# Optimization experiments

Hardware: AMD Instinct MI355X
Metric: run time of the kernel (lower is better)

## Reference

```python
import jax, jax.numpy as jnp
import numpy as np

N_HEADS = 16


def setup_inputs() -> dict:
    key = jax.random.key(0)
    ks = jax.random.split(key, 8)
    B, S, E = 4, 2048, 1024
    s = 0.02
    return {
        "input_tensor": jax.random.normal(ks[0], (B, S, E), jnp.float32),
        "mask": jnp.zeros((B, 1, 1, S), jnp.float32),  # additive mask (0 = keep)
        "WQ_w": jax.random.normal(ks[1], (E, E), jnp.float32) * s,
        "WQ_b": jnp.zeros((E,), jnp.float32),
        "WK_w": jax.random.normal(ks[2], (E, E), jnp.float32) * s,
        "WK_b": jnp.zeros((E,), jnp.float32),
        "WV_w": jax.random.normal(ks[3], (E, E), jnp.float32) * s,
        "WV_b": jnp.zeros((E,), jnp.float32),
        "WO_w": jax.random.normal(ks[4], (E, E), jnp.float32) * s,
        "WO_b": jnp.zeros((E,), jnp.float32),
        "ln_w": jnp.ones((E,), jnp.float32),
        "ln_b": jnpp if False else jnp.zeros((E,), jnp.float32),
    }


def reference(input_tensor, mask, WQ_w, WQ_b, WK_w, WK_b, WV_w, WV_b,
              WO_w, WO_b, ln_w, ln_b):
    B, S, E = input_tensor.shape
    H = N_HEADS
    D = E // H
    scale = jnp.sqrt(jnp.asarray(D, input_tensor.dtype))

    def split_heads(x):  # [B,S,E] -> [B,H,S,D]
        return x.reshape(B, S, H, D).transpose(0, 2, 1, 3)

    q = split_heads(input_tensor @ WQ_w.T + WQ_b)
    k = split_heads(input_tensor @ WK_w.T + WK_b)
    v = split_heads(input_tensor @ WV_w.T + WV_b)

    scores = jnp.einsum("bhqd,bhkd->bhqk", q, k) / scale + mask
    probs = jax.nn.softmax(scores, axis=-1)  # attn dropout is identity in eval
    ctx = jnp.einsum("bhqk,bhkd->bhqd", probs, v)
    ctx = ctx.transpose(0, 2, 1, 3).reshape(B, S, E)

    out = ctx @ WO_w.T + WO_b  # out dropout is identity in eval
    x = input_tensor + out
    mu = jnp.mean(x, axis=-1, keepdims=True)
    var = jnp.var(x, axis=-1, keepdims=True)
    eps = 1e-12
    return (x - mu) * jax.lax.rsqrt(var + eps) * ln_w + ln_b
```

## Files before the change

### kernel.cpp

```cpp
#include <hip/hip_runtime.h>
#include <hip/hip_bf16.h>
#include <stdint.h>


typedef short bf16x8_t __attribute__((ext_vector_type(8)));
typedef float f32x4_t __attribute__((ext_vector_type(4)));
typedef float f32x16_t __attribute__((ext_vector_type(16)));
typedef unsigned short u16x8_t __attribute__((ext_vector_type(8)));
typedef uint32_t u32x4_t __attribute__((ext_vector_type(4)));

#define DEV static __device__ __forceinline__

DEV unsigned short f2bf(float f) {
  union { float f; uint32_t u; } v; v.f = f;
  uint32_t u = v.u;
  return (unsigned short)((u + 0x7fffu + ((u >> 16) & 1u)) >> 16);
}

DEV uint32_t cvtpk(float a, float b) {
  uint32_t d;
  asm("v_cvt_pk_bf16_f32 %0, %1, %2" : "=v"(d) : "v"(a), "v"(b));
  return d;
}

DEV void plswap(uint32_t& a, uint32_t& b) {
  asm("v_permlane32_swap_b32 %0, %1" : "+v"(a), "+v"(b));
}

DEV float ex2(float x) { return __builtin_amdgcn_exp2f(x); }

template<int N> DEV void wait_vm() {
  asm volatile("s_waitcnt vmcnt(%0)" :: "n"(N) : "memory");
}
DEV void bar() { __builtin_amdgcn_s_barrier(); }
DEV void sbar0() { __builtin_amdgcn_sched_barrier(0); }

typedef const __attribute__((address_space(1))) void* gp_t;
typedef __attribute__((address_space(3))) void* lp_t;

DEV void gld16(const void* g, void* l) {
  __builtin_amdgcn_global_load_lds((gp_t)g, (lp_t)l, 16, 0, 0);
}

__global__ __launch_bounds__(256) void cast_all(
    const float* __restrict__ x,
    const float* __restrict__ wq, const float* __restrict__ wk,
    const float* __restrict__ wv, const float* __restrict__ wo,
    const float* __restrict__ mask,
    unsigned short* __restrict__ xb,
    unsigned short* __restrict__ wqb, unsigned short* __restrict__ wkb,
    unsigned short* __restrict__ wvb, unsigned short* __restrict__ wob,
    float* __restrict__ emf, unsigned short* __restrict__ emb)
{
  const int cid = blockIdx.x;
  if (cid >= 6144) {
    int i = ((cid - 6144) * 256 + (int)threadIdx.x) * 8;
    float4 a = *(const float4*)(mask + i);
    float4 b = *(const float4*)(mask + i + 4);
    const float C = 1.44269504f;
    float4 ea, eb;
    ea.x = ex2(a.x * C); ea.y = ex2(a.y * C); ea.z = ex2(a.z * C); ea.w = ex2(a.w * C);
    eb.x = ex2(b.x * C); eb.y = ex2(b.y * C); eb.z = ex2(b.z * C); eb.w = ex2(b.w * C);
    *(float4*)(emf + i) = ea;
    *(float4*)(emf + i + 4) = eb;
    u16x8_t o;
    o[0] = f2bf(ea.x); o[1] = f2bf(ea.y); o[2] = f2bf(ea.z); o[3] = f2bf(ea.w);
    o[4] = f2bf(eb.x); o[5] = f2bf(eb.y); o[6] = f2bf(eb.z); o[7] = f2bf(eb.w);
    *(u16x8_t*)(emb + i) = o;
    return;
  }
  const float* src; unsigned short* dst; int base;
  if (cid < 4096)      { src = x;  dst = xb;  base = cid; }
  else if (cid < 4608) { src = wq; dst = wqb; base = cid - 4096; }
  else if (cid < 5120) { src = wk; dst = wkb; base = cid - 4608; }
  else if (cid < 5632) { src = wv; dst = wvb; base = cid - 5120; }
  else                 { src = wo; dst = wob; base = cid - 5632; }
  int i = (base * 256 + (int)threadIdx.x) * 8;
  float4 a = *(const float4*)(src + i);
  float4 b = *(const float4*)(src + i + 4);
  u16x8_t o;
  o[0] = f2bf(a.x); o[1] = f2bf(a.y); o[2] = f2bf(a.z); o[3] = f2bf(a.w);
  o[4] = f2bf(b.x); o[5] = f2bf(b.y); o[6] = f2bf(b.z); o[7] = f2bf(b.w);
  *(u16x8_t*)(dst + i) = o;
}

template<int MODE>
__global__ __launch_bounds__(256) void gemm_bt(
    const unsigned short* __restrict__ A,
    const unsigned short* __restrict__ B0, const unsigned short* __restrict__ B1,
    const float* __restrict__ bias0, const float* __restrict__ bias1,
    const float* __restrict__ resid,
    unsigned short* __restrict__ o0, unsigned short* __restrict__ o1,
    float* __restrict__ of,
    int M, int N, int K)
{
  __shared__ unsigned short As[2][128 * 32];
  __shared__ unsigned short Bs[2][128 * 32];

  const int z = blockIdx.z;
  const unsigned short* Bw = (MODE == 0 && z == 1) ? B1 : B0;
  const float* bias = (MODE == 0 && z == 1) ? bias1 : bias0;
  unsigned short* obf = (MODE == 0 && z == 1) ? o1 : o0;

  const int tid = threadIdx.x;
  const int lane = tid & 63;
  const int lr = lane & 15, lq = lane >> 4;
  const int wid = tid >> 6;
  const int m0 = blockIdx.x * 128;
  const int n0 = blockIdx.y * 128;
  const int wr = (wid >> 1) * 64, wc = (wid & 1) * 64;

  f32x4_t acc[4][4] = {};

  const int o = tid * 16;
  const int srow = o >> 6, scb = o & 63;

  auto STAGE = [&](int kt, int p) {
#pragma unroll
    for (int r = 0; r < 2; ++r) {
      int row = srow + r * 64;
      int oo = o + r * 4096;
      gld16((const char*)(A  + (size_t)(m0 + row) * K + kt) + scb, (char*)As[p] + oo);
      gld16((const char*)(Bw + (size_t)(n0 + row) * K + kt) + scb, (char*)Bs[p] + oo);
    }
  };

  STAGE(0, 0);
  wait_vm<0>();
  bar(); sbar0();

  int cur = 0;
  for (int kt = 32; kt <= K; kt += 32) {
    if (kt < K) {
      STAGE(kt, cur ^ 1);
      wait_vm<4>();
    } else {
      wait_vm<0>();
    }
    bar(); sbar0();

    bf16x8_t aF[4], bF[4];
    const int koff = lq * 16;
#pragma unroll
    for (int i = 0; i < 4; ++i) {
      aF[i] = *(const bf16x8_t*)((const char*)As[cur] + (wr + i * 16 + lr) * 64 + koff);
      bF[i] = *(const bf16x8_t*)((const char*)Bs[cur] + (wc + i * 16 + lr) * 64 + koff);
    }
#pragma unroll
    for (int i = 0; i < 4; ++i)
#pragma unroll
      for (int j = 0; j < 4; ++j)
        acc[i][j] = __builtin_amdgcn_mfma_f32_16x16x32_bf16(aF[i], bF[j], acc[i][j], 0, 0, 0);

    bar();
    cur ^= 1;
  }

#pragma unroll
  for (int i = 0; i < 4; ++i) {
#pragma unroll
    for (int j = 0; j < 4; ++j) {
      int n = n0 + wc + j * 16 + lr;
#pragma unroll
      for (int r = 0; r < 4; ++r) {
        int m = m0 + wr + i * 16 + lq * 4 + r;
        float v = acc[i][j][r];
        if (MODE == 0) {
          v = (v + bias[n]) * (z == 0 ? 0.18033688f : 1.0f);
          int b = m >> 11, s = m & 2047, h = n >> 6, d = n & 63;
          obf[(size_t)((b * 16 + h) * 2048 + s) * 64 + d] = f2bf(v);
        } else if (MODE == 2) {
          v = (v + bias[m]) * resid[n];
          int b = n >> 11, s = n & 2047;
          obf[(size_t)(b * 1024 + m) * 2048 + s] = f2bf(v);
        } else {
          v = v + bias[n] + resid[(size_t)m * 1024 + n];
          of[(size_t)m * 1024 + n] = v;
        }
      }
    }
  }
}

__global__ __launch_bounds__(256, 2) void attn_kernel(
    const unsigned short* __restrict__ Qg, const unsigned short* __restrict__ Kg,
    const unsigned short* __restrict__ Vtg, const unsigned short* __restrict__ EMb,
    unsigned short* __restrict__ ctx)
{
  __shared__ __align__(16) char smem[69632];

  const int id = blockIdx.x;
  const int swz = (id & 7) * 64 + (id >> 3);
  const int bh = swz >> 3, qt = swz & 7;
  const int b = bh >> 4, h = bh & 15;

  const int tid = threadIdx.x, lane = tid & 63, wid = tid >> 6;
  const int l31 = lane & 31, hi = lane >> 5;
  const int q0 = qt * 256 + wid * 64;
  const size_t head = (size_t)bh * (2048 * 64);
  const unsigned short* Kh = Kg + head;
  const unsigned short* Vh = Vtg + (size_t)bh * 64 * 2048;
  const unsigned short* emrow = EMb + (size_t)b * 2048;

  bf16x8_t qf[2][4];
#pragma unroll
  for (int qg = 0; qg < 2; ++qg) {
    const unsigned short* qp = Qg + head + (size_t)(q0 + qg * 32 + l31) * 64 + 8 * hi;
#pragma unroll
    for (int ds = 0; ds < 4; ++ds) qf[qg][ds] = *(const bf16x8_t*)(qp + ds * 16);
  }

  f32x16_t oaccA[2] = {}, oaccB[2] = {};
  f32x16_t lacc[2] = {};

  const int sw_row = (l31 & 7) << 4;

  auto STAGE = [&](int t, int p) {
    const int k0 = t * 128;
    char* kd = smem + p * 16384;
    char* vd = smem + 32768 + p * 16384;
#pragma unroll
    for (int r = 0; r < 4; ++r) {
      int oo = tid * 16 + r * 4096;
      {
        int row = oo >> 7, cb = oo & 127;
        int scb = cb ^ ((row & 7) << 4);
        gld16((const char*)(Kh + (size_t)(k0 + row) * 64) + scb, kd + oo);
      }
      {
        int row = oo >> 8, cb = oo & 255;
        int scb = cb ^ ((row & 7) << 4);
        gld16((const char*)(Vh + (size_t)row * 2048 + k0) + scb, vd + oo);
      }
    }
  };

  gld16((const char*)(emrow + tid * 8), smem + 65536 + tid * 16);
  STAGE(0, 0);
  wait_vm<0>();
  bar(); sbar0();

  for (int t = 0; t < 16; ++t) {
    const int p = t & 1;
    if (t < 15) {
      STAGE(t + 1, p ^ 1);
      wait_vm<8>();
    } else {
      wait_vm<0>();
    }
    bar(); sbar0();

    const char* kb = smem + p * 16384;
    const char* vb = smem + 32768 + p * 16384;
    const char* eb = smem + 65536 + t * 256;

#pragma unroll
    for (int s = 0; s < 2; ++s) {
      f32x16_t c0[2] = {}, c1[2] = {};
      {
        const char* kr0 = kb + s * 8192 + l31 * 128;
        const char* kr1 = kb + s * 8192 + (32 + l31) * 128;
        __builtin_amdgcn_s_setprio(1);
#pragma unroll
        for (int ds = 0; ds < 4; ++ds) {
          int cc = (ds * 32 + 16 * hi) ^ sw_row;
          bf16x8_t k0f = *(const bf16x8_t*)(kr0 + cc);
          bf16x8_t k1f = *(const bf16x8_t*)(kr1 + cc);
#pragma unroll
          for (int qg = 0; qg < 2; ++qg) {
            c0[qg] = __builtin_amdgcn_mfma_f32_32x32x16_bf16(k0f, qf[qg][ds], c0[qg], 0, 0, 0);
            c1[qg] = __builtin_amdgcn_mfma_f32_32x32x16_bf16(k1f, qf[qg][ds], c1[qg], 0, 0, 0);
          }
        }
        __builtin_amdgcn_s_setprio(0);
      }

      bf16x8_t pf[2][4];
#pragma unroll
      for (int qg = 0; qg < 2; ++qg) {
        uint32_t w0[8], w1[8];
#pragma unroll
        for (int g = 0; g < 8; ++g) {
          const int i4 = (g & 3) * 4;
          if (g < 4) {
            w0[g] = cvtpk(ex2(c0[qg][i4]), ex2(c0[qg][i4 + 1]));
            w1[g] = cvtpk(ex2(c0[qg][i4 + 2]), ex2(c0[qg][i4 + 3]));
          } else {
            w0[g] = cvtpk(ex2(c1[qg][i4]), ex2(c1[qg][i4 + 1]));
            w1[g] = cvtpk(ex2(c1[qg][i4 + 2]), ex2(c1[qg][i4 + 3]));
          }
        }
#pragma unroll
        for (int ks = 0; ks < 4; ++ks) {
          const int gg = ((ks >> 1) << 2) + ((ks & 1) << 1);
          uint32_t a0 = w0[gg], b0 = w0[gg + 1];
          uint32_t a1 = w1[gg], b1 = w1[gg + 1];
          plswap(a0, b0);
          plswap(a1, b1);
          union { uint32_t u[4]; bf16x8_t v; } cv;
          cv.u[0] = a0; cv.u[1] = a1; cv.u[2] = b0; cv.u[3] = b1;
          pf[qg][ks] = cv.v;
        }
      }

      {
        const char* vr0 = vb + l31 * 256 + s * 128;
        const char* vr1 = vb + (32 + l31) * 256 + s * 128;
        const char* ebs = eb + s * 128;
        __builtin_amdgcn_s_setprio(1);
#pragma unroll
        for (int ks = 0; ks < 4; ++ks) {
          bf16x8_t ef = *(const bf16x8_t*)(ebs + ks * 32 + 16 * hi);
          int cc = (ks * 32 + 16 * hi) ^ sw_row;
          bf16x8_t v0f = *(const bf16x8_t*)(vr0 + cc);
          bf16x8_t v1f = *(const bf16x8_t*)(vr1 + cc);
#pragma unroll
          for (int qg = 0; qg < 2; ++qg) {
            oaccA[qg] = __builtin_amdgcn_mfma_f32_32x32x16_bf16(v0f, pf[qg][ks], oaccA[qg], 0, 0, 0);
            oaccB[qg] = __builtin_amdgcn_mfma_f32_32x32x16_bf16(v1f, pf[qg][ks], oaccB[qg], 0, 0, 0);
            lacc[qg]  = __builtin_amdgcn_mfma_f32_32x32x16_bf16(ef,  pf[qg][ks], lacc[qg],  0, 0, 0);
          }
        }
        __builtin_amdgcn_s_setprio(0);
      }
    }
    bar();
  }

  char* tb = smem + wid * 8192;
#pragma unroll
  for (int qg = 0; qg < 2; ++qg) {
    const float inv = 1.0f / lacc[qg][0];
    char* trow = tb + qg * 4096 + l31 * 128;
    const int swq = (l31 & 7) << 4;
#pragma unroll
    for (int g2 = 0; g2 < 4; ++g2) {
      uint2 a0, a1;
      a0.x = cvtpk(oaccA[qg][4 * g2] * inv, oaccA[qg][4 * g2 + 1] * inv);
      a0.y = cvtpk(oaccA[qg][4 * g2 + 2] * inv, oaccA[qg][4 * g2 + 3] * inv);
      a1.x = cvtpk(oaccB[qg][4 * g2] * inv, oaccB[qg][4 * g2 + 1] * inv);
      a1.y = cvtpk(oaccB[qg][4 * g2 + 2] * inv, oaccB[qg][4 * g2 + 3] * inv);
      int d0 = 16 * g2 + 8 * hi;
      *(uint2*)(trow + ((d0) ^ swq)) = a0;
      *(uint2*)(trow + ((d0 + 64) ^ swq)) = a1;
    }
  }
#pragma unroll
  for (int half = 0; half < 2; ++half) {
    const int qq = half * 32 + (lane >> 1), cp = lane & 1;
    const char* trow = tb + qq * 128;
    const int swr = (qq & 7) << 4;
    unsigned short* op = ctx + ((size_t)(b * 2048 + q0 + qq)) * 1024 + h * 64 + cp * 32;
#pragma unroll
    for (int i = 0; i < 4; ++i) {
      int col = cp * 64 + i * 16;
      u32x4_t val = *(const u32x4_t*)(trow + (col ^ swr));
      *(u32x4_t*)(op + i * 8) = val;
    }
  }
}

__global__ __launch_bounds__(256) void ln_kernel(
    float* __restrict__ y, const float* __restrict__ g, const float* __restrict__ be)
{
  const int row = blockIdx.x, tid = threadIdx.x;
  float* rp = y + (size_t)row * 1024;
  float4 x = *(const float4*)(rp + tid * 4);
  float s = x.x + x.y + x.z + x.w;
  float sq = x.x * x.x + x.y * x.y + x.z * x.z + x.w * x.w;
#pragma unroll
  for (int msk = 1; msk < 64; msk <<= 1) {
    s  += __shfl_xor(s, msk);
    sq += __shfl_xor(sq, msk);
  }
  __shared__ float red[8];
  const int wid = tid >> 6, lane = tid & 63;
  if (lane == 0) { red[wid] = s; red[4 + wid] = sq; }
  __syncthreads();
  s  = red[0] + red[1] + red[2] + red[3];
  sq = red[4] + red[5] + red[6] + red[7];
  float mu = s * (1.f / 1024.f);
  float var = sq * (1.f / 1024.f) - mu * mu;
  float rs = rsqrtf(var + 1e-12f);
  float4 gw = *(const float4*)(g + tid * 4);
  float4 bw = *(const float4*)(be + tid * 4);
  float4 o2;
  o2.x = (x.x - mu) * rs * gw.x + bw.x;
  o2.y = (x.y - mu) * rs * gw.y + bw.y;
  o2.z = (x.z - mu) * rs * gw.z + bw.z;
  o2.w = (x.w - mu) * rs * gw.w + bw.w;
  *(float4*)(rp + tid * 4) = o2;
}

extern "C" void kernel_launch(void* const* d_in, const int* in_sizes, int n_in,
                              void* d_out, int out_size, void* d_ws, size_t ws_size,
                              hipStream_t stream)
{
  const float* x    = (const float*)d_in[0];
  const float* mask = (const float*)d_in[1];
  const float* wq   = (const float*)d_in[2];
  const float* bq   = (const float*)d_in[3];
  const float* wk   = (const float*)d_in[4];
  const float* bk   = (const float*)d_in[5];
  const float* wv   = (const float*)d_in[6];
  const float* bv   = (const float*)d_in[7];
  const float* wo   = (const float*)d_in[8];
  const float* bo   = (const float*)d_in[9];
  const float* lnw  = (const float*)d_in[10];
  const float* lnb  = (const float*)d_in[11];
  float* out = (float*)d_out;

  char* ws = (char*)d_ws;
  unsigned short* Xb  = (unsigned short*)(ws);
  unsigned short* Wqb = (unsigned short*)(ws + 16777216);
  unsigned short* Wkb = (unsigned short*)(ws + 16777216 + 2097152);
  unsigned short* Wvb = (unsigned short*)(ws + 16777216 + 2 * 2097152);
  unsigned short* Wob = (unsigned short*)(ws + 16777216 + 3 * 2097152);
  unsigned short* Qg  = (unsigned short*)(ws + 25165824);
  unsigned short* Kg  = (unsigned short*)(ws + 25165824 + 16777216);
  unsigned short* Vtg = (unsigned short*)(ws + 25165824 + 2 * 16777216);
  unsigned short* CTX = (unsigned short*)(ws + 25165824 + 3 * 16777216);
  float*          EMf = (float*)(ws + 92274688);
  unsigned short* EMb = (unsigned short*)(ws + 92274688 + 32768);

  cast_all<<<dim3(6148), 256, 0, stream>>>(x, wq, wk, wv, wo, mask,
                                           Xb, Wqb, Wkb, Wvb, Wob, EMf, EMb);
  gemm_bt<0><<<dim3(64, 8, 2), 256, 0, stream>>>(Xb, Wqb, Wkb, bq, bk, nullptr,
                                                 Qg, Kg, nullptr, 8192, 1024, 1024);
  gemm_bt<2><<<dim3(8, 64, 1), 256, 0, stream>>>(Wvb, Xb, nullptr, bv, nullptr, EMf,
                                                 Vtg, nullptr, nullptr, 1024, 8192, 1024);
  attn_kernel<<<dim3(512), 256, 0, stream>>>(Qg, Kg, Vtg, EMb, CTX);
  gemm_bt<3><<<dim3(64, 8, 1), 256, 0, stream>>>(CTX, Wob, nullptr, bo, nullptr, x,
                                                 nullptr, nullptr, out, 8192, 1024, 1024);
  ln_kernel<<<dim3(8192), 256, 0, stream>>>(out, lnw, lnb);
}
```

Measured before the change: 215.4 us.

## Enlarge GEMM tiles to 256x128 with 512 threads and 3-stage swizzled LDS pipeline

Reworks the shared bf16 GEMM kernel to use 256x128 output tiles with 8 waves per block, a K-step of 64, and a triple-buffered LDS pipeline that prefetches two stages ahead. LDS rows use an XOR swizzle to avoid bank conflicts on the 128-byte row stride. Grids for the Q/K, V and output projections are halved in the M dimension to match. The intent is more data reuse per load and deeper latency hiding. The cost is about 144KB of LDS per block, which likely limits each CU to one block, plus a tail wave on the Q/K launch.

```diff
diff --git a/kernel.cpp b/kernel.cpp
--- a/kernel.cpp
+++ b/kernel.cpp
@@ -85,7 +85,7 @@
 }
 
 template<int MODE>
-__global__ __launch_bounds__(256) void gemm_bt(
+__global__ __launch_bounds__(512, 2) void gemm_bt(
     const unsigned short* __restrict__ A,
     const unsigned short* __restrict__ B0, const unsigned short* __restrict__ B1,
     const float* __restrict__ bias0, const float* __restrict__ bias1,
@@ -94,8 +94,7 @@
     float* __restrict__ of,
     int M, int N, int K)
 {
-  __shared__ unsigned short As[2][128 * 32];
-  __shared__ unsigned short Bs[2][128 * 32];
+  __shared__ __align__(16) char smem[147456];
 
   const int z = blockIdx.z;
   const unsigned short* Bw = (MODE == 0 && z == 1) ? B1 : B0;
@@ -106,64 +105,79 @@
   const int lane = tid & 63;
   const int lr = lane & 15, lq = lane >> 4;
   const int wid = tid >> 6;
-  const int m0 = blockIdx.x * 128;
+  const int wm = wid >> 2, wn = wid & 3;
+  const int m0 = blockIdx.x * 256;
   const int n0 = blockIdx.y * 128;
-  const int wr = (wid >> 1) * 64, wc = (wid & 1) * 64;
-
-  f32x4_t acc[4][4] = {};
-
-  const int o = tid * 16;
-  const int srow = o >> 6, scb = o & 63;
+
+  f32x4_t acc[8][2] = {};
 
   auto STAGE = [&](int kt, int p) {
-#pragma unroll
-    for (int r = 0; r < 2; ++r) {
-      int row = srow + r * 64;
-      int oo = o + r * 4096;
-      gld16((const char*)(A  + (size_t)(m0 + row) * K + kt) + scb, (char*)As[p] + oo);
-      gld16((const char*)(Bw + (size_t)(n0 + row) * K + kt) + scb, (char*)Bs[p] + oo);
+    char* ad = smem + p * 32768;
+    char* bd = smem + 98304 + p * 16384;
+    const int ke = kt * 64;
+#pragma unroll
+    for (int l = 0; l < 4; ++l) {
+      int oo = tid * 16 + l * 8192;
+      int row = oo >> 7, cb = oo & 127;
+      int scb = cb ^ ((row & 7) << 4);
+      gld16((const char*)(A + (size_t)(m0 + row) * K + ke) + scb, ad + oo);
+    }
+#pragma unroll
+    for (int l = 0; l < 2; ++l) {
+      int oo = tid * 16 + l * 8192;
+      int row = oo >> 7, cb = oo & 127;
+      int scb = cb ^ ((row & 7) << 4);
+      gld16((const char*)(Bw + (size_t)(n0 + row) * K + ke) + scb, bd + oo);
     }
   };
 
+  const int NT = K >> 6;
   STAGE(0, 0);
-  wait_vm<0>();
+  STAGE(1, 1);
+  wait_vm<6>();
   bar(); sbar0();
 
-  int cur = 0;
-  for (int kt = 32; kt <= K; kt += 32) {
-    if (kt < K) {
-      STAGE(kt, cur ^ 1);
-      wait_vm<4>();
-    } else {
-      wait_vm<0>();
-    }
+  for (int t = 0; t < NT; ++t) {
+    const int p = t % 3;
+    if (t + 2 < NT) { STAGE(t + 2, (t + 2) % 3); wait_vm<6>(); }
+    else if (t == NT - 1) { wait_vm<0>(); }
+    else { wait_vm<6>(); }
     bar(); sbar0();
 
-    bf16x8_t aF[4], bF[4];
-    const int koff = lq * 16;
-#pragma unroll
-    for (int i = 0; i < 4; ++i) {
-      aF[i] = *(const bf16x8_t*)((const char*)As[cur] + (wr + i * 16 + lr) * 64 + koff);
-      bF[i] = *(const bf16x8_t*)((const char*)Bs[cur] + (wc + i * 16 + lr) * 64 + koff);
-    }
-#pragma unroll
-    for (int i = 0; i < 4; ++i)
-#pragma unroll
-      for (int j = 0; j < 4; ++j)
-        acc[i][j] = __builtin_amdgcn_mfma_f32_16x16x32_bf16(aF[i], bF[j], acc[i][j], 0, 0, 0);
-
+    const char* ab = smem + p * 32768;
+    const char* bb = smem + 98304 + p * 16384;
+#pragma unroll
+    for (int ks = 0; ks < 2; ++ks) {
+      bf16x8_t aF[8], bF[2];
+#pragma unroll
+      for (int i = 0; i < 8; ++i) {
+        int row = wm * 128 + i * 16 + lr;
+        int cc = (ks * 64 + lq * 16) ^ ((row & 7) << 4);
+        aF[i] = *(const bf16x8_t*)(ab + row * 128 + cc);
+      }
+#pragma unroll
+      for (int j = 0; j < 2; ++j) {
+        int row = wn * 32 + j * 16 + lr;
+        int cc = (ks * 64 + lq * 16) ^ ((row & 7) << 4);
+        bF[j] = *(const bf16x8_t*)(bb + row * 128 + cc);
+      }
+#pragma unroll
+      for (int i = 0; i < 8; ++i)
+#pragma unroll
+        for (int j = 0; j < 2; ++j)
+          acc[i][j] = __builtin_amdgcn_mfma_f32_16x16x32_bf16(aF[i], bF[j], acc[i][j], 0, 0, 0);
+    }
     bar();
-    cur ^= 1;
-  }
-
-#pragma unroll
-  for (int i = 0; i < 4; ++i) {
-#pragma unroll
-    for (int j = 0; j < 4; ++j) {
-      int n = n0 + wc + j * 16 + lr;
+  }
+
+#pragma unroll
+  for (int i = 0; i < 8; ++i) {
+#pragma unroll
+    for (int j = 0; j < 2; ++j) {
+      int n = n0 + wn * 32 + j * 16 + lr;
 #pragma unroll
       for (int r = 0; r < 4; ++r) {
-        int m = m0 + wr + i * 16 + lq * 4 + r;
+        int m = m0 + wm * 128 + i * 16 + lq * 4 + r;
         float v = acc[i][j][r];
         if (MODE == 0) {
           v = (v + bias[n]) * (z == 0 ? 0.18033688f : 1.0f);
@@ -425,12 +439,12 @@
 
   cast_all<<<dim3(6148), 256, 0, stream>>>(x, wq, wk, wv, wo, mask,
                                            Xb, Wqb, Wkb, Wvb, Wob, EMf, EMb);
-  gemm_bt<0><<<dim3(64, 8, 2), 256, 0, stream>>>(Xb, Wqb, Wkb, bq, bk, nullptr,
+  gemm_bt<0><<<dim3(32, 8, 2), 512, 0, stream>>>(Xb, Wqb, Wkb, bq, bk, nullptr,
                                                  Qg, Kg, nullptr, 8192, 1024, 1024);
-  gemm_bt<2><<<dim3(8, 64, 1), 256, 0, stream>>>(Wvb, Xb, nullptr, bv, nullptr, EMf,
+  gemm_bt<2><<<dim3(4, 64, 1), 512, 0, stream>>>(Wvb, Xb, nullptr, bv, nullptr, EMf,
                                                  Vtg, nullptr, nullptr, 1024, 8192, 1024);
   attn_kernel<<<dim3(512), 256, 0, stream>>>(Qg, Kg, Vtg, EMb, CTX);
-  gemm_bt<3><<<dim3(64, 8, 1), 256, 0, stream>>>(CTX, Wob, nullptr, bo, nullptr, x,
+  gemm_bt<3><<<dim3(32, 8, 1), 512, 0, stream>>>(CTX, Wob, nullptr, bo, nullptr, x,
                                                  nullptr, nullptr, out, 8192, 1024, 1024);
   ln_kernel<<<dim3(8192), 256, 0, stream>>>(out, lnw, lnb);
 }
```

Result: faster. 201.6 us (-6.4%).
